# Kernel optimization log

Hardware: AMD Instinct MI355X
Metric: run time of the kernel (lower is better)

Reference implementation:

```python
import jax, jax.numpy as jnp
import numpy as np

B, T, NCH, DFF = 64, 480, 32, 32   # batch, seq_len+pred_len, d_model, d_ff
LAYERS = 3                          # conv_layers
NFFT, WIN, HOP = 64, 64, 4
FRAMES = T // HOP + 1               # 121 == (seq_len+pred_len+hop)/hop


def _stft(x):
    # x: [B, N, T] real -> (re, im) each [B, N, NFFT, FRAMES]
    # torch.stft(center=True, pad_mode='reflect', normalized=True, onesided=False)
    pad = NFFT // 2
    xp = jnp.pad(x, ((0, 0), (0, 0), (pad, pad)), mode='reflect')
    idx = jnp.arange(FRAMES)[:, None] * HOP + jnp.arange(NFFT)[None, :]
    win = 0.5 * (1.0 - jnp.cos(2.0 * jnp.pi * jnp.arange(WIN, dtype=jnp.float32) / WIN))  # periodic hann
    frames = xp[:, :, idx] * win                      # [B, N, FRAMES, NFFT]
    spec = jnp.fft.fft(frames, axis=-1) / jnp.sqrt(jnp.float32(NFFT))
    spec = jnp.swapaxes(spec, -1, -2)                 # [B, N, NFFT, FRAMES]
    return spec.real.astype(x.dtype), spec.imag.astype(x.dtype)


def _conv2d(x, w, b, dil, pad):
    y = jax.lax.conv_general_dilated(
        x, w, window_strides=(1, 1), padding=[(pad, pad), (pad, pad)],
        rhs_dilation=(dil, dil), dimension_numbers=('NCHW', 'OIHW', 'NCHW'))
    return y + b[None, :, None, None]


def _cconv(xr, xi, wr, wi, br, bi, dil, pad):
    # apply_complexConv2D: fr(re) - fi(im) + 1j*(fr(im) + fi(re)), biases included in each apply
    rr = _conv2d(xr, wr, br, dil, pad)
    ri = _conv2d(xi, wr, br, dil, pad)
    ir = _conv2d(xr, wi, bi, dil, pad)
    ii = _conv2d(xi, wi, bi, dil, pad)
    return rr - ii, ri + ir


def _cmul(order, ar, ai, br, bi):
    return (jnp.einsum(order, ar, br) - jnp.einsum(order, ai, bi),
            jnp.einsum(order, ar, bi) + jnp.einsum(order, ai, br))


def reference(x, w0r, w0i, b0r, b0i, W1r, W1i, B1r, B1i, W2r, W2i, B2r, B2i, w_l0, b_l0, w_l2, b_l2):
    xt = jnp.swapaxes(x, 1, 2)                         # [B, N, T]
    sr, si = _stft(xt)                                 # [B, N, F, K]
    qkr, qki = _cmul('bnfk,bngk->bnfg', sr, si, sr, si)
    qkr, qki = jax.nn.sigmoid(qkr), jax.nn.sigmoid(qki)
    ar, ai = _cmul('bnfg,bngk->bnfk', qkr, qki, sr, si)

    outs_r, outs_i = [], []
    r0, i0 = _cconv(ar, ai, w0r, w0i, b0r, b0i, 1, 0)  # 1x1 complex conv
    outs_r.append(jax.nn.relu(r0)); outs_i.append(jax.nn.relu(i0))
    for k in range(1, LAYERS):                          # dilated 3x3 complex conv pairs
        j = k - 1
        hr, hi = _cconv(ar, ai, W1r[j], W1i[j], B1r[j], B1i[j], k, k)
        hr, hi = _cconv(hr, hi, W2r[j], W2i[j], B2r[j], B2i[j], k, k)
        outs_r.append(jax.nn.relu(hr)); outs_i.append(jax.nn.relu(hi))
    mr = sum(outs_r) / LAYERS
    mi = sum(outs_i) / LAYERS

    # l0: Linear(2 -> 1) over stacked [real, imag]
    cr = mr * w_l0[0, 0] + mi * w_l0[0, 1] + b_l0[0]    # [B, N, F, K]
    h = cr.mean(axis=2)                                 # [B, N, K]
    y = jnp.einsum('bnk,tk->bnt', h, w_l2) + b_l2       # l2: Linear(FRAMES -> T)
    return jnp.transpose(y, (0, 2, 1))                  # [B, T, N]


def setup_inputs() -> dict:
    key = jax.random.key(0)
    ks = jax.random.split(key, 18)
    s1 = 1.0 / np.sqrt(NCH)          # 1x1 conv fan-in
    s3 = 1.0 / np.sqrt(NCH * 9)      # 3x3 conv fan-in
    return {
        'x':   jax.random.normal(ks[0], (B, T, NCH), jnp.float32),
        'w0r': jax.random.normal(ks[1], (NCH, NCH, 1, 1), jnp.float32) * s1,
        'w0i': jax.random.normal(ks[2], (NCH, NCH, 1, 1), jnp.float32) * s1,
        'b0r': jax.random.normal(ks[3], (NCH,), jnp.float32) * 0.01,
        'b0i': jax.random.normal(ks[4], (NCH,), jnp.float32) * 0.01,
        'W1r': jax.random.normal(ks[5], (LAYERS - 1, DFF, NCH, 3, 3), jnp.float32) * s3,
        'W1i': jax.random.normal(ks[6], (LAYERS - 1, DFF, NCH, 3, 3), jnp.float32) * s3,
        'B1r': jax.random.normal(ks[7], (LAYERS - 1, DFF), jnp.float32) * 0.01,
        'B1i': jax.random.normal(ks[8], (LAYERS - 1, DFF), jnp.float32) * 0.01,
        'W2r': jax.random.normal(ks[9], (LAYERS - 1, NCH, DFF, 3, 3), jnp.float32) * s3,
        'W2i': jax.random.normal(ks[10], (LAYERS - 1, NCH, DFF, 3, 3), jnp.float32) * s3,
        'B2r': jax.random.normal(ks[11], (LAYERS - 1, NCH), jnp.float32) * 0.01,
        'B2i': jax.random.normal(ks[12], (LAYERS - 1, NCH), jnp.float32) * 0.01,
        'w_l0': jax.random.normal(ks[13], (1, 2), jnp.float32) * 0.5,
        'b_l0': jax.random.normal(ks[14], (1,), jnp.float32) * 0.01,
        'w_l2': jax.random.normal(ks[15], (T, FRAMES), jnp.float32) * (1.0 / np.sqrt(FRAMES)),
        'b_l2': jax.random.normal(ks[16], (T,), jnp.float32) * 0.01,
    }
```

## Files before the change

### kernel.cpp

```cpp
#include <hip/hip_runtime.h>
#include <hip/hip_bf16.h>


typedef __attribute__((ext_vector_type(8))) short bf16x8;
typedef __attribute__((ext_vector_type(4))) short bf16x4;
typedef __attribute__((ext_vector_type(4))) float f32x4;

__device__ __forceinline__ ushort f2bf(float v) {
  __hip_bfloat16 h = __float2bfloat16(v);
  return *reinterpret_cast<ushort*>(&h);
}
__device__ __forceinline__ float bf2f_raw(ushort u) {
  union { uint i; float f; } c; c.i = ((uint)u) << 16; return c.f;
}
__device__ __forceinline__ void split_bf(float v, ushort& h, ushort& l) {
  h = f2bf(v); l = f2bf(v - bf2f_raw(h));
}
__device__ __forceinline__ bf16x8 mk8(bf16x4 a, bf16x4 b) {
  bf16x8 r;
  r[0]=a[0]; r[1]=a[1]; r[2]=a[2]; r[3]=a[3];
  r[4]=b[0]; r[5]=b[1]; r[6]=b[2]; r[7]=b[3];
  return r;
}

#define MFMA16(A,B,C) __builtin_amdgcn_mfma_f32_16x16x32_bf16(A, B, C, 0, 0, 0)
#define SPMACC(acc, Ah, Al, Bh, Bl)      \
  acc = MFMA16(Ah, Bh, acc);             \
  acc = MFMA16(Al, Bh, acc);             \
  acc = MFMA16(Ah, Bl, acc);

__global__ __launch_bounds__(512) void stft_mfma_k(const float* __restrict__ x,
                                                   const ushort* __restrict__ WF,
                                                   ushort* __restrict__ ap) {
  __shared__ __align__(16) char smem[133376];
  const int bid = blockIdx.x;
  const int b = bid >> 5, n = bid & 31;
  const int tid = threadIdx.x;
  ushort* xph = reinterpret_cast<ushort*>(smem + 131072);
  ushort* xpl = xph + 576;

  for (int i = tid; i < 576; i += 512) {
    float v = 0.f;
    if (i < 544) {
      int p = i - 32;
      if (p < 0) p = -p;
      if (p >= 480) p = 958 - p;
      v = x[(b * 480 + p) * 32 + n];
    }
    ushort h, l; split_bf(v, h, l);
    xph[i] = h; xpl[i] = l;
  }
  __syncthreads();

  const int wv = tid >> 6, lane = tid & 63;
  const int mt = wv >> 1, nth = wv & 1;
  const int l15 = lane & 15, l4 = lane >> 4;

  bf16x8 WA[2][2][2];
#pragma unroll
  for (int cs = 0; cs < 2; ++cs)
#pragma unroll
    for (int part = 0; part < 2; ++part)
#pragma unroll
      for (int ks = 0; ks < 2; ++ks)
        WA[cs][part][ks] = *reinterpret_cast<const bf16x8*>(
            WF + (((cs * 2 + part) * 2 + ks) * 4 + mt) * 512 + lane * 8);

  f32x4 acc1[2][4];
#pragma unroll
  for (int cs = 0; cs < 2; ++cs)
#pragma unroll
    for (int nt = 0; nt < 4; ++nt) acc1[cs][nt] = (f32x4){0.f, 0.f, 0.f, 0.f};

#pragma unroll
  for (int ks = 0; ks < 2; ++ks) {
    bf16x8 bh[4], bl[4];
#pragma unroll
    for (int nt = 0; nt < 4; ++nt) {
      int n_ = ((nth * 4 + nt) * 16) + l15;
      int e = n_ * 4 + ks * 32 + l4 * 8;
      bf16x4 h0 = *reinterpret_cast<const bf16x4*>(xph + e);
      bf16x4 h1 = *reinterpret_cast<const bf16x4*>(xph + e + 4);
      bf16x4 l0 = *reinterpret_cast<const bf16x4*>(xpl + e);
      bf16x4 l1 = *reinterpret_cast<const bf16x4*>(xpl + e + 4);
      bh[nt] = mk8(h0, h1); bl[nt] = mk8(l0, l1);
    }
#pragma unroll
    for (int cs = 0; cs < 2; ++cs)
#pragma unroll
      for (int nt = 0; nt < 4; ++nt) {
        SPMACC(acc1[cs][nt], WA[cs][0][ks], WA[cs][1][ks], bh[nt], bl[nt]);
      }
  }

#pragma unroll
  for (int cs = 0; cs < 2; ++cs)
#pragma unroll
    for (int nt = 0; nt < 4; ++nt) {
      int k = (nth * 4 + nt) * 16 + l15;
      bool kv = (k < 121);
#pragma unroll
      for (int r = 0; r < 4; ++r) {
        int f = mt * 16 + l4 * 4 + r;
        float v = kv ? acc1[cs][nt][r] : 0.f;
        ushort h, l; split_bf(v, h, l);
        int ba = (f << 8) + (k << 1); ba ^= (f & 7) << 4;
        *reinterpret_cast<ushort*>(smem + cs * 32768 + ba) = h;
        *reinterpret_cast<ushort*>(smem + cs * 32768 + 16384 + ba) = l;
        int bt = (k << 7) + (f << 1); bt ^= (k & 7) << 4;
        *reinterpret_cast<ushort*>(smem + 65536 + cs * 32768 + bt) = h;
        *reinterpret_cast<ushort*>(smem + 65536 + cs * 32768 + 16384 + bt) = l;
      }
    }
  __syncthreads();

  f32x4 acc2[2][4];
#pragma unroll
  for (int nt = 0; nt < 2; ++nt)
#pragma unroll
    for (int c = 0; c < 4; ++c) acc2[nt][c] = (f32x4){0.f, 0.f, 0.f, 0.f};

#pragma unroll
  for (int ks = 0; ks < 4; ++ks) {
    bf16x8 A_[2][2];
#pragma unroll
    for (int comp = 0; comp < 2; ++comp)
#pragma unroll
      for (int part = 0; part < 2; ++part) {
        int f = mt * 16 + l15;
        int ba = (f << 8) + ((ks * 32 + l4 * 8) << 1); ba ^= (f & 7) << 4;
        A_[comp][part] = *reinterpret_cast<const bf16x8*>(smem + comp * 32768 + part * 16384 + ba);
      }
    bf16x8 B_[2][2][2];
#pragma unroll
    for (int comp = 0; comp < 2; ++comp)
#pragma unroll
      for (int part = 0; part < 2; ++part)
#pragma unroll
        for (int nt = 0; nt < 2; ++nt) {
          int g = (nth * 2 + nt) * 16 + l15;
          int ba = (g << 8) + ((ks * 32 + l4 * 8) << 1); ba ^= (g & 7) << 4;
          B_[comp][part][nt] = *reinterpret_cast<const bf16x8*>(smem + comp * 32768 + part * 16384 + ba);
        }
#pragma unroll
    for (int nt = 0; nt < 2; ++nt) {
      SPMACC(acc2[nt][0], A_[0][0], A_[0][1], B_[0][0][nt], B_[0][1][nt]);
      SPMACC(acc2[nt][1], A_[1][0], A_[1][1], B_[1][0][nt], B_[1][1][nt]);
      SPMACC(acc2[nt][2], A_[0][0], A_[0][1], B_[1][0][nt], B_[1][1][nt]);
      SPMACC(acc2[nt][3], A_[1][0], A_[1][1], B_[0][0][nt], B_[0][1][nt]);
    }
  }
  __syncthreads();

#pragma unroll
  for (int nt = 0; nt < 2; ++nt) {
    int g = (nth * 2 + nt) * 16 + l15;
#pragma unroll
    for (int r = 0; r < 4; ++r) {
      int f = mt * 16 + l4 * 4 + r;
      float qr = acc2[nt][0][r] - acc2[nt][1][r];
      float qi = acc2[nt][2][r] + acc2[nt][3][r];
      float vr = 1.f / (1.f + __expf(-qr));
      float vi = 1.f / (1.f + __expf(-qi));
      int ba = (f << 7) + (g << 1); ba ^= (f & 7) << 4;
      ushort h, l;
      split_bf(vr, h, l);
      *reinterpret_cast<ushort*>(smem + ba) = h;
      *reinterpret_cast<ushort*>(smem + 8192 + ba) = l;
      split_bf(vi, h, l);
      *reinterpret_cast<ushort*>(smem + 16384 + ba) = h;
      *reinterpret_cast<ushort*>(smem + 24576 + ba) = l;
    }
  }
  __syncthreads();

  f32x4 acc3[4][3];
#pragma unroll
  for (int nt = 0; nt < 4; ++nt)
#pragma unroll
    for (int c = 0; c < 3; ++c) acc3[nt][c] = (f32x4){0.f, 0.f, 0.f, 0.f};

#pragma unroll
  for (int ks = 0; ks < 2; ++ks) {
    bf16x8 QA[2][2];
#pragma unroll
    for (int comp = 0; comp < 2; ++comp)
#pragma unroll
      for (int part = 0; part < 2; ++part) {
        int f = mt * 16 + l15;
        int ba = (f << 7) + ((ks * 32 + l4 * 8) << 1); ba ^= (f & 7) << 4;
        QA[comp][part] = *reinterpret_cast<const bf16x8*>(smem + comp * 16384 + part * 8192 + ba);
      }
#pragma unroll
    for (int nt = 0; nt < 4; ++nt) {
      int k = (nth * 4 + nt) * 16 + l15;
      int bq = (k << 7) + ((ks * 32 + l4 * 8) << 1); bq ^= (k & 7) << 4;
      bf16x8 Srh = *reinterpret_cast<const bf16x8*>(smem + 65536 + bq);
      bf16x8 Srl = *reinterpret_cast<const bf16x8*>(smem + 81920 + bq);
      bf16x8 Sih = *reinterpret_cast<const bf16x8*>(smem + 98304 + bq);
      bf16x8 Sil = *reinterpret_cast<const bf16x8*>(smem + 114688 + bq);
      SPMACC(acc3[nt][0], QA[0][0], QA[0][1], Srh, Srl);
      SPMACC(acc3[nt][1], QA[1][0], QA[1][1], Sih, Sil);
      SPMACC(acc3[nt][2], QA[0][0], QA[0][1], Sih, Sil);
      SPMACC(acc3[nt][2], QA[1][0], QA[1][1], Srh, Srl);
    }
  }
  __syncthreads();

#pragma unroll
  for (int nt = 0; nt < 4; ++nt) {
    int k = (nth * 4 + nt) * 16 + l15;
#pragma unroll
    for (int r = 0; r < 4; ++r) {
      int f = mt * 16 + l4 * 4 + r;
      float ar = acc3[nt][0][r] - acc3[nt][1][r];
      float ai = acc3[nt][2][r];
      int ba = (f << 8) + (k << 1); ba ^= (f & 7) << 4;
      *reinterpret_cast<ushort*>(smem + ba) = f2bf(ar);
      *reinterpret_cast<ushort*>(smem + 16384 + ba) = f2bf(ai);
    }
  }
  __syncthreads();

  uint4* dst = reinterpret_cast<uint4*>(ap);
  for (int i = tid; i < 2048; i += 512) {
    int comp = i >> 10, rem = i & 1023;
    int f = rem >> 4, q = rem & 15;
    uint4 v = *reinterpret_cast<const uint4*>(
        smem + comp * 16384 + (f << 8) + ((q ^ (f & 7)) << 4));
    dst[((size_t)(b * 64 + n + 32 * comp) * 64) * 16 + rem] = v;
  }
}

__global__ __launch_bounds__(256) void transpose_k(const ushort* __restrict__ ap,
                                                   ushort* __restrict__ an) {
  __shared__ ushort T[64 * 128];
  const int b = blockIdx.x >> 6, h = blockIdx.x & 63;
  const int tid = threadIdx.x;
#pragma unroll
  for (int it = 0; it < 4; ++it) {
    int i = it * 256 + tid;
    int cc = i >> 4, q = i & 15;
    const uint4* src = reinterpret_cast<const uint4*>(ap) +
                       ((size_t)((b * 64 + cc) * 64 + h) * 16 + q);
    *reinterpret_cast<uint4*>(&T[cc * 128 + q * 8]) = *src;
  }
  __syncthreads();
  const int p = tid >> 1, cc0 = (tid & 1) * 32;
  uint ou[16];
#pragma unroll
  for (int it = 0; it < 16; ++it) {
    uint lo = T[(cc0 + 2 * it) * 128 + p];
    uint hi = T[(cc0 + 2 * it + 1) * 128 + p];
    ou[it] = lo | (hi << 16);
  }
  uint4* dst = reinterpret_cast<uint4*>(an + ((size_t)((b * 64 + h) * 128 + p) * 64 + cc0));
#pragma unroll
  for (int r = 0; r < 4; ++r) dst[r] = make_uint4(ou[4*r], ou[4*r+1], ou[4*r+2], ou[4*r+3]);
}

__global__ __launch_bounds__(256) void prep_k(
    const float* __restrict__ w0r, const float* __restrict__ w0i,
    const float* __restrict__ b0r, const float* __restrict__ b0i,
    const float* __restrict__ W1r, const float* __restrict__ W1i,
    const float* __restrict__ B1r, const float* __restrict__ B1i,
    const float* __restrict__ W2r, const float* __restrict__ W2i,
    const float* __restrict__ B2r, const float* __restrict__ B2i,
    const float* __restrict__ wl2,
    ushort* __restrict__ AF, ushort* __restrict__ WF, float* __restrict__ BB,
    float* __restrict__ wl2T) {
  const int blk = blockIdx.x, tid = threadIdx.x;
  const float PI32 = 0.0981747704246810387f;

  if (blk == 38) {
    for (int i = tid; i < 121 * 480; i += 256) {
      int k = i / 480, t = i - k * 480;
      wl2T[i] = wl2[t * 121 + k];
    }
    return;
  }
  if (blk == 37) {
    for (int i = tid; i < 16384; i += 256) {
      int j = i & 7, ln = (i >> 3) & 63, mt = (i >> 9) & 3, ks = (i >> 11) & 1;
      int part = (i >> 12) & 1, cs = (i >> 13) & 1;
      int f = mt * 16 + (ln & 15);
      int t = ks * 32 + (ln >> 4) * 8 + j;
      float win = 0.5f * (1.0f - __cosf(PI32 * (float)t));
      int m = (f * t) & 63;
      float sv, cv;
      __sincosf(PI32 * (float)m, &sv, &cv);
      float val = (cs == 0) ? (win * cv * 0.125f) : (-win * sv * 0.125f);
      ushort h = f2bf(val);
      WF[i] = part ? f2bf(val - bf2f_raw(h)) : h;
    }
    return;
  }

  int conv, tap, TT;
  const float *Wr, *Wi;
  if (blk == 0) { conv = 0; tap = 0; TT = 1; Wr = w0r; Wi = w0i; }
  else {
    int q = blk - 1; conv = 1 + q / 9; tap = q - (q / 9) * 9; TT = 9;
    if (conv == 1)      { Wr = W1r;        Wi = W1i; }
    else if (conv == 2) { Wr = W2r;        Wi = W2i; }
    else if (conv == 3) { Wr = W1r + 9216; Wi = W1i + 9216; }
    else                { Wr = W2r + 9216; Wi = W2i + 9216; }
  }
  ushort thi[16], tlo[16];
#pragma unroll
  for (int jj = 0; jj < 16; ++jj) {
    int e = tid * 16 + jj;
    int j = e & 7, lane_e = (e >> 3) & 63, mt = (e >> 9) & 3, ks = (e >> 11) & 1;
    int o  = mt * 16 + (lane_e & 15);
    int cc = ks * 32 + 8 * (lane_e >> 4) + j;
    int ci = cc & 31, ch = cc >> 5, on = o & 31, oh = o >> 5;
    float wr = Wr[(on * 32 + ci) * TT + tap];
    float wi = Wi[(on * 32 + ci) * TT + tap];
    float v = (oh == 0) ? (ch == 0 ? wr : -wi) : (ch == 0 ? wi : wr);
    ushort h = f2bf(v);
    thi[jj] = h;
    tlo[jj] = f2bf(v - bf2f_raw(h));
  }
  ushort* base = AF + conv * 73728 + tap * 8192 + tid * 16;
  uint4* dh = reinterpret_cast<uint4*>(base);
  uint4* dl = reinterpret_cast<uint4*>(base + 4096);
  dh[0] = *reinterpret_cast<uint4*>(&thi[0]);
  dh[1] = *reinterpret_cast<uint4*>(&thi[8]);
  dl[0] = *reinterpret_cast<uint4*>(&tlo[0]);
  dl[1] = *reinterpret_cast<uint4*>(&tlo[8]);

  if (blk == 0) {
    for (int i = tid; i < 320; i += 256) {
      int c = i >> 6, o = i & 63;
      const float *br, *bi;
      if (c == 0)      { br = b0r;      bi = b0i; }
      else if (c == 1) { br = B1r;      bi = B1i; }
      else if (c == 2) { br = B2r;      bi = B2i; }
      else if (c == 3) { br = B1r + 32; bi = B1i + 32; }
      else             { br = B2r + 32; bi = B2i + 32; }
      BB[c * 64 + o] = (o < 32) ? (br[o] - bi[o]) : (br[o - 32] + bi[o - 32]);
    }
  }
}

#define RWB 8704

template <int NT>
__device__ __forceinline__ void run_taps(const char* __restrict__ smem,
    const ushort* __restrict__ afrag, int d,
    int ng, int mtb, int l15, int l4, int lane, f32x4 acc[2][8]) {
  const ushort* Ab = afrag + lane * 8;
#pragma unroll
  for (int t = 0; t < NT; ++t) {
    const int dy = (NT == 1) ? 1 : (t / 3);
    const int dxo = ((NT == 1) ? 0 : ((t - (t / 3) * 3) - 1)) * d;
    const int bufb = (dy - 1) * d + 2 + ng * 2;
    const ushort* At = Ab + t * 8192;
    bf16x8 AH[2][2], AL[2][2];
#pragma unroll
    for (int ks = 0; ks < 2; ++ks)
#pragma unroll
      for (int mi = 0; mi < 2; ++mi) {
        AH[ks][mi] = *reinterpret_cast<const bf16x8*>(At + ks * 2048 + (mtb + 2 * mi) * 512);
        AL[ks][mi] = *reinterpret_cast<const bf16x8*>(At + 4096 + ks * 2048 + (mtb + 2 * mi) * 512);
      }
#pragma unroll
    for (int ks = 0; ks < 2; ++ks) {
      bf16x8 bv[8];
#pragma unroll
      for (int nt = 0; nt < 8; ++nt) {
        int bw = (nt & 3) * 16 + l15 + dxo + 2;
        int byt = (bufb + (nt >> 2)) * RWB + bw * 128 + ks * 64 + l4 * 16;
        byt ^= (bw & 7) << 4;
        bv[nt] = *reinterpret_cast<const bf16x8*>(smem + byt);
      }
      __builtin_amdgcn_s_setprio(1);
#pragma unroll
      for (int nt = 0; nt < 8; ++nt) {
        acc[0][nt] = MFMA16(AH[ks][0], bv[nt], acc[0][nt]);
        acc[1][nt] = MFMA16(AH[ks][1], bv[nt], acc[1][nt]);
      }
#pragma unroll
      for (int nt = 0; nt < 8; ++nt) {
        acc[0][nt] = MFMA16(AL[ks][0], bv[nt], acc[0][nt]);
        acc[1][nt] = MFMA16(AL[ks][1], bv[nt], acc[1][nt]);
      }
      __builtin_amdgcn_s_setprio(0);
    }
  }
}

template <int ROWS>
__device__ __forceinline__ void conv_body(char* smem,
    const ushort* __restrict__ xin, ushort* __restrict__ tout,
    const ushort* __restrict__ afrag, const float* __restrict__ bb,
    const float* __restrict__ wl0, float* __restrict__ csum,
    int d, int b, int h0, int side, int mode, int tid) {
  const int wave = tid >> 6, lane = tid & 63;
  const int mtb = wave & 1;
  const int ng = wave >> 1;
  const int l15 = lane & 15, l4 = lane >> 4;
  const int wbase = side * 64;

  const int RSTG = (ROWS == 1) ? 4 : 8;
#pragma unroll
  for (int r = 0; r < RSTG; ++r) {
    const int hh = (ROWS == 1) ? (h0 + r) : (h0 + r - 2);
    const int buf = (ROWS == 1) ? (r + 2) : r;
    const bool hv = ((unsigned)hh < 64u);
    uint4 st[3];
#pragma unroll
    for (int c = 0; c < 3; ++c) {
      int i = c * 256 + tid;
      uint4 v = make_uint4(0u, 0u, 0u, 0u);
      if (i < 544) {
        int bw = i >> 3, q = i & 7;
        int gw = wbase + bw - 2;
        if (hv && (unsigned)gw < 128u)
          v = *reinterpret_cast<const uint4*>(
              xin + (((size_t)(b * 64 + hh) * 128 + gw) * 64 + q * 8));
      }
      st[c] = v;
    }
#pragma unroll
    for (int c = 0; c < 3; ++c) {
      int i = c * 256 + tid;
      if (i < 544) {
        int bw = i >> 3, q = i & 7;
        int byt = buf * RWB + bw * 128 + q * 16;
        byt ^= (bw & 7) << 4;
        *reinterpret_cast<uint4*>(smem + byt) = st[c];
      }
    }
  }
  __syncthreads();

  f32x4 acc[2][8];
#pragma unroll
  for (int mi = 0; mi < 2; ++mi)
#pragma unroll
    for (int nt = 0; nt < 8; ++nt) acc[mi][nt] = (f32x4){0.f, 0.f, 0.f, 0.f};

  run_taps<(ROWS == 1) ? 1 : 9>(smem, afrag, d, ng, mtb, l15, l4, lane, acc);

  if (mode == 2) {
    __syncthreads();
    uint* Lb = reinterpret_cast<uint*>(smem);
#pragma unroll
    for (int mi = 0; mi < 2; ++mi) {
#pragma unroll
      for (int rp = 0; rp < 2; ++rp) {
        int o = (mtb + 2 * mi) * 16 + l4 * 4 + rp * 2;
        float b0 = bb[o], b1 = bb[o + 1];
#pragma unroll
        for (int nt = 0; nt < 8; ++nt) {
          int jrow = ng * 2 + (nt >> 2);
          int wl = (nt & 3) * 16 + l15;
          uint pk = (uint)f2bf(acc[mi][nt][rp * 2] + b0) |
                    ((uint)f2bf(acc[mi][nt][rp * 2 + 1] + b1) << 16);
          Lb[(jrow * 32 + (o >> 1)) * 66 + wl] = pk;
        }
      }
    }
    __syncthreads();
#pragma unroll
    for (int c = 0; c < 8; ++c) {
      int i = c * 256 + tid;
      int jrow = i >> 9, rem = i & 511;
      int wl = rem >> 3, q = rem & 7;
      int gw = wbase + wl;
      int hh = h0 + jrow;
      bool val = (gw < 121);
      uint4 v;
      v.x = val ? Lb[(jrow * 32 + q * 4 + 0) * 66 + wl] : 0u;
      v.y = val ? Lb[(jrow * 32 + q * 4 + 1) * 66 + wl] : 0u;
      v.z = val ? Lb[(jrow * 32 + q * 4 + 2) * 66 + wl] : 0u;
      v.w = val ? Lb[(jrow * 32 + q * 4 + 3) * 66 + wl] : 0u;
      *reinterpret_cast<uint4*>(
          tout + (((size_t)(b * 64 + hh) * 128 + gw) * 64 + q * 8)) = v;
    }
  } else {
    const float w00 = wl0[0], w01 = wl0[1];
#pragma unroll
    for (int nt = 0; nt < 8; ++nt) {
      int gw = wbase + (nt & 3) * 16 + l15;
      int hh = h0 + ng * 2 + (nt >> 2);
      if (gw < 121) {
#pragma unroll
        for (int r = 0; r < 4; ++r) {
          int n = mtb * 16 + l4 * 4 + r;
          float rr = acc[0][nt][r] + bb[n];
          float im = acc[1][nt][r] + bb[n + 32];
          float v = (fmaxf(rr, 0.f) * w00 + fmaxf(im, 0.f) * w01) * (1.f / 3.f);
          float* p = csum + ((size_t)(b * 32 + n) * 64 + hh) * 121 + gw;
          if (mode == 1) v += *p;
          *p = v;
        }
      }
    }
  }
}

__global__ __launch_bounds__(256, 2) void convD1_k(
    const ushort* __restrict__ an, ushort* __restrict__ t1, ushort* __restrict__ t2,
    const ushort* __restrict__ AF, const float* __restrict__ BB,
    const float* __restrict__ wl0, float* __restrict__ csumA) {
  __shared__ __align__(16) char smem[8 * RWB];
  const int x = blockIdx.x & 7, j = blockIdx.x >> 3;
  const int role = j % 3, sub = j / 3;
  const int wg = (x << 8) | sub;
  const int b = wg >> 5, rem = wg & 31;
  const int h0 = ((rem >> 1) & 15) * 4, side = rem & 1;
  const int tid = threadIdx.x;
  if (role == 0)
    conv_body<1>(smem, an, nullptr, AF, BB, wl0, csumA, 1, b, h0, side, 0, tid);
  else if (role == 1)
    conv_body<3>(smem, an, t1, AF + 1 * 73728, BB + 64, wl0, nullptr, 1, b, h0, side, 2, tid);
  else
    conv_body<3>(smem, an, t2, AF + 3 * 73728, BB + 192, wl0, nullptr, 2, b, h0, side, 2, tid);
}

__global__ __launch_bounds__(256, 2) void convD2_k(
    const ushort* __restrict__ t1, const ushort* __restrict__ t2,
    const ushort* __restrict__ AF, const float* __restrict__ BB,
    const float* __restrict__ wl0, float* __restrict__ csumA,
    float* __restrict__ csumB) {
  __shared__ __align__(16) char smem[8 * RWB];
  const int x = blockIdx.x & 7, j = blockIdx.x >> 3;
  const int role = j & 1, sub = j >> 1;
  const int wg = (x << 8) | sub;
  const int b = wg >> 5, rem = wg & 31;
  const int h0 = ((rem >> 1) & 15) * 4, side = rem & 1;
  const int tid = threadIdx.x;
  if (role == 0)
    conv_body<3>(smem, t1, nullptr, AF + 2 * 73728, BB + 128, wl0, csumA, 1, b, h0, side, 1, tid);
  else
    conv_body<3>(smem, t2, nullptr, AF + 4 * 73728, BB + 256, wl0, csumB, 2, b, h0, side, 0, tid);
}

__global__ __launch_bounds__(256) void epi_k(const float* __restrict__ csumA,
    const float* __restrict__ csumB,
    const float* __restrict__ bl0, const float* __restrict__ wl2T,
    const float* __restrict__ bl2, float* __restrict__ out) {
  const int b = blockIdx.x >> 5, n = blockIdx.x & 31;
  __shared__ float sh[121];
  const int tid = threadIdx.x;
  const float* baseA = csumA + (size_t)(b * 32 + n) * 64 * 121;
  const float* baseB = csumB + (size_t)(b * 32 + n) * 64 * 121;
  for (int k = tid; k < 121; k += 256) {
    float s = 0.f;
#pragma unroll 8
    for (int f = 0; f < 64; ++f) s += baseA[f * 121 + k] + baseB[f * 121 + k];
    sh[k] = s * (1.f / 64.f) + bl0[0];
  }
  __syncthreads();
  for (int t = tid; t < 480; t += 256) {
    float acc = bl2[t];
#pragma unroll 8
    for (int k = 0; k < 121; ++k) acc = fmaf(sh[k], wl2T[k * 480 + t], acc);
    out[(b * 480 + t) * 32 + n] = acc;
  }
}

extern "C" void kernel_launch(void* const* d_in, const int* in_sizes, int n_in,
                              void* d_out, int out_size, void* d_ws, size_t ws_size,
                              hipStream_t stream) {
  const float* x   = (const float*)d_in[0];
  const float* w0r = (const float*)d_in[1];
  const float* w0i = (const float*)d_in[2];
  const float* b0r = (const float*)d_in[3];
  const float* b0i = (const float*)d_in[4];
  const float* W1r = (const float*)d_in[5];
  const float* W1i = (const float*)d_in[6];
  const float* B1r = (const float*)d_in[7];
  const float* B1i = (const float*)d_in[8];
  const float* W2r = (const float*)d_in[9];
  const float* W2i = (const float*)d_in[10];
  const float* B2r = (const float*)d_in[11];
  const float* B2i = (const float*)d_in[12];
  const float* wl0 = (const float*)d_in[13];
  const float* bl0 = (const float*)d_in[14];
  const float* wl2 = (const float*)d_in[15];
  const float* bl2 = (const float*)d_in[16];

  char* ws = (char*)d_ws;
  const size_t MB64 = (size_t)64 << 20;
  ushort* ap    = (ushort*)ws;
  ushort* t2    = (ushort*)ws;
  ushort* an    = (ushort*)(ws + MB64);
  float*  csumB = (float*)(ws + MB64);
  ushort* t1    = (ushort*)(ws + 2 * MB64);
  float*  csumA = (float*)(ws + 3 * MB64);
  const size_t CSZ = (size_t)64 * 32 * 64 * 121 * 4;
  ushort* AF   = (ushort*)(ws + 3 * MB64 + CSZ);
  ushort* WFp  = AF + 5 * 73728;
  float*  BB   = (float*)(WFp + 16384);
  float*  wl2T = BB + 320;
  float*  out  = (float*)d_out;

  hipLaunchKernelGGL(prep_k, dim3(39), dim3(256), 0, stream,
                     w0r, w0i, b0r, b0i, W1r, W1i, B1r, B1i, W2r, W2i, B2r, B2i,
                     wl2, AF, WFp, BB, wl2T);
  hipLaunchKernelGGL(stft_mfma_k, dim3(2048), dim3(512), 0, stream, x, WFp, ap);
  hipLaunchKernelGGL(transpose_k, dim3(4096), dim3(256), 0, stream, ap, an);
  hipLaunchKernelGGL(convD1_k, dim3(6144), dim3(256), 0, stream,
                     an, t1, t2, AF, BB, wl0, csumA);
  hipLaunchKernelGGL(convD2_k, dim3(4096), dim3(256), 0, stream,
                     t1, t2, AF, BB, wl0, csumA, csumB);
  hipLaunchKernelGGL(epi_k, dim3(2048), dim3(256), 0, stream,
                     csumA, csumB, bl0, wl2T, bl2, out);
}
```

Measured before the change: 555.9 us.

## Make conv kernels persistent with rolling row buffer and fuse 1x1 conv into transpose

The 1x1 complex conv is moved into the transpose kernel, reusing the transposed tile already in shared memory to compute its csum contribution. The 3x3 conv kernels become persistent: each block walks 32 rows using a ring of 8 shared-memory row buffers, prefetching the next 4 rows into registers while computing. Weight fragments for the next tap are double-buffered in registers. This removes the redundant halo reloads and cuts launch overhead, at the cost of only 512 blocks (less parallelism) and higher register pressure.

New measurement: 1.058 ms. 90.3% more time.

```diff
diff --git a/kernel.cpp b/kernel.cpp
--- a/kernel.cpp
+++ b/kernel.cpp
@@ -233,8 +233,10 @@
 }
 
 __global__ __launch_bounds__(256) void transpose_k(const ushort* __restrict__ ap,
-                                                   ushort* __restrict__ an) {
-  __shared__ ushort T[64 * 128];
+    ushort* __restrict__ an, const ushort* __restrict__ AF,
+    const float* __restrict__ BB, const float* __restrict__ wl0,
+    float* __restrict__ csumA) {
+  __shared__ __align__(16) ushort T[64 * 128];
   const int b = blockIdx.x >> 6, h = blockIdx.x & 63;
   const int tid = threadIdx.x;
 #pragma unroll
@@ -257,6 +259,70 @@
   uint4* dst = reinterpret_cast<uint4*>(an + ((size_t)((b * 64 + h) * 128 + p) * 64 + cc0));
 #pragma unroll
   for (int r = 0; r < 4; ++r) dst[r] = make_uint4(ou[4*r], ou[4*r+1], ou[4*r+2], ou[4*r+3]);
+  __syncthreads();
+
+  char* S = reinterpret_cast<char*>(T);
+#pragma unroll
+  for (int it = 0; it < 16; ++it) {
+    int byt = p * 128 + (cc0 + 2 * it) * 2;
+    byt ^= (p & 7) << 4;
+    *reinterpret_cast<uint*>(S + byt) = ou[it];
+  }
+  __syncthreads();
+
+  const int wave = tid >> 6, lane = tid & 63;
+  const int mtb = wave & 1, ntb = (wave >> 1) * 4;
+  const int l15 = lane & 15, l4 = lane >> 4;
+  const ushort* Ab = AF + lane * 8;
+  bf16x8 AH[2][2], AL[2][2];
+#pragma unroll
+  for (int ks = 0; ks < 2; ++ks)
+#pragma unroll
+    for (int mi = 0; mi < 2; ++mi) {
+      AH[ks][mi] = *reinterpret_cast<const bf16x8*>(Ab + ks * 2048 + (mtb + 2 * mi) * 512);
+      AL[ks][mi] = *reinterpret_cast<const bf16x8*>(Ab + 4096 + ks * 2048 + (mtb + 2 * mi) * 512);
+    }
+  f32x4 acc[2][4];
+#pragma unroll
+  for (int mi = 0; mi < 2; ++mi)
+#pragma unroll
+    for (int nt = 0; nt < 4; ++nt) acc[mi][nt] = (f32x4){0.f, 0.f, 0.f, 0.f};
+#pragma unroll
+  for (int ks = 0; ks < 2; ++ks) {
+    bf16x8 bv[4];
+#pragma unroll
+    for (int nt = 0; nt < 4; ++nt) {
+      int w = (ntb + nt) * 16 + l15;
+      int byt = w * 128 + ks * 64 + l4 * 16;
+      byt ^= (w & 7) << 4;
+      bv[nt] = *reinterpret_cast<const bf16x8*>(S + byt);
+    }
+#pragma unroll
+    for (int nt = 0; nt < 4; ++nt) {
+      acc[0][nt] = MFMA16(AH[ks][0], bv[nt], acc[0][nt]);
+      acc[1][nt] = MFMA16(AH[ks][1], bv[nt], acc[1][nt]);
+    }
+#pragma unroll
+    for (int nt = 0; nt < 4; ++nt) {
+      acc[0][nt] = MFMA16(AL[ks][0], bv[nt], acc[0][nt]);
+      acc[1][nt] = MFMA16(AL[ks][1], bv[nt], acc[1][nt]);
+    }
+  }
+  const float w00 = wl0[0], w01 = wl0[1];
+#pragma unroll
+  for (int nt = 0; nt < 4; ++nt) {
+    int gw = (ntb + nt) * 16 + l15;
+    if (gw < 121) {
+#pragma unroll
+      for (int r = 0; r < 4; ++r) {
+        int n = mtb * 16 + l4 * 4 + r;
+        float rr = acc[0][nt][r] + BB[n];
+        float im = acc[1][nt][r] + BB[n + 32];
+        csumA[((size_t)(b * 32 + n) * 64 + h) * 121 + gw] =
+            (fmaxf(rr, 0.f) * w00 + fmaxf(im, 0.f) * w01) * (1.f / 3.f);
+      }
+    }
+  }
 }
 
 __global__ __launch_bounds__(256) void prep_k(
@@ -345,179 +411,235 @@
 
 #define RWB 8704
 
-template <int NT>
-__device__ __forceinline__ void run_taps(const char* __restrict__ smem,
-    const ushort* __restrict__ afrag, int d,
+__device__ __forceinline__ void run9(const char* __restrict__ smem,
+    const ushort* __restrict__ afrag, bf16x8 AC[2][2][2], int d, int h0,
     int ng, int mtb, int l15, int l4, int lane, f32x4 acc[2][8]) {
   const ushort* Ab = afrag + lane * 8;
-#pragma unroll
-  for (int t = 0; t < NT; ++t) {
-    const int dy = (NT == 1) ? 1 : (t / 3);
-    const int dxo = ((NT == 1) ? 0 : ((t - (t / 3) * 3) - 1)) * d;
-    const int bufb = (dy - 1) * d + 2 + ng * 2;
-    const ushort* At = Ab + t * 8192;
-    bf16x8 AH[2][2], AL[2][2];
-#pragma unroll
-    for (int ks = 0; ks < 2; ++ks)
-#pragma unroll
-      for (int mi = 0; mi < 2; ++mi) {
-        AH[ks][mi] = *reinterpret_cast<const bf16x8*>(At + ks * 2048 + (mtb + 2 * mi) * 512);
-        AL[ks][mi] = *reinterpret_cast<const bf16x8*>(At + 4096 + ks * 2048 + (mtb + 2 * mi) * 512);
-      }
+  bf16x8 AN[2][2][2];
+#pragma unroll
+  for (int t = 0; t < 9; ++t) {
+    if (t < 8) {
+      const ushort* At = Ab + (t + 1) * 8192;
+#pragma unroll
+      for (int pp = 0; pp < 2; ++pp)
+#pragma unroll
+        for (int ks = 0; ks < 2; ++ks)
+#pragma unroll
+          for (int mi = 0; mi < 2; ++mi)
+            AN[pp][ks][mi] = *reinterpret_cast<const bf16x8*>(
+                At + pp * 4096 + ks * 2048 + (mtb + 2 * mi) * 512);
+    }
+    const int dy = t / 3;
+    const int dxo = (t - dy * 3 - 1) * d;
+    const int bufb = h0 + (dy - 1) * d + 2 + ng * 2;
+    const int base0 = (bufb & 7) * RWB;
+    const int base1 = ((bufb + 1) & 7) * RWB;
 #pragma unroll
     for (int ks = 0; ks < 2; ++ks) {
       bf16x8 bv[8];
 #pragma unroll
       for (int nt = 0; nt < 8; ++nt) {
         int bw = (nt & 3) * 16 + l15 + dxo + 2;
-        int byt = (bufb + (nt >> 2)) * RWB + bw * 128 + ks * 64 + l4 * 16;
+        int byt = ((nt >> 2) ? base1 : base0) + bw * 128 + ks * 64 + l4 * 16;
         byt ^= (bw & 7) << 4;
         bv[nt] = *reinterpret_cast<const bf16x8*>(smem + byt);
       }
       __builtin_amdgcn_s_setprio(1);
 #pragma unroll
       for (int nt = 0; nt < 8; ++nt) {
-        acc[0][nt] = MFMA16(AH[ks][0], bv[nt], acc[0][nt]);
-        acc[1][nt] = MFMA16(AH[ks][1], bv[nt], acc[1][nt]);
+        acc[0][nt] = MFMA16(AC[0][ks][0], bv[nt], acc[0][nt]);
+        acc[1][nt] = MFMA16(AC[0][ks][1], bv[nt], acc[1][nt]);
       }
 #pragma unroll
       for (int nt = 0; nt < 8; ++nt) {
-        acc[0][nt] = MFMA16(AL[ks][0], bv[nt], acc[0][nt]);
-        acc[1][nt] = MFMA16(AL[ks][1], bv[nt], acc[1][nt]);
+        acc[0][nt] = MFMA16(AC[1][ks][0], bv[nt], acc[0][nt]);
+        acc[1][nt] = MFMA16(AC[1][ks][1], bv[nt], acc[1][nt]);
       }
       __builtin_amdgcn_s_setprio(0);
     }
-  }
-}
-
-template <int ROWS>
-__device__ __forceinline__ void conv_body(char* smem,
+    if (t < 8) {
+#pragma unroll
+      for (int pp = 0; pp < 2; ++pp)
+#pragma unroll
+        for (int ks = 0; ks < 2; ++ks)
+#pragma unroll
+          for (int mi = 0; mi < 2; ++mi)
+            AC[pp][ks][mi] = AN[pp][ks][mi];
+    }
+  }
+}
+
+__device__ __forceinline__ void conv_persist(char* __restrict__ smem,
     const ushort* __restrict__ xin, ushort* __restrict__ tout,
     const ushort* __restrict__ afrag, const float* __restrict__ bb,
     const float* __restrict__ wl0, float* __restrict__ csum,
-    int d, int b, int h0, int side, int mode, int tid) {
+    int d, int b, int side, int hbase, int mode, int tid) {
   const int wave = tid >> 6, lane = tid & 63;
   const int mtb = wave & 1;
   const int ng = wave >> 1;
   const int l15 = lane & 15, l4 = lane >> 4;
   const int wbase = side * 64;
-
-  const int RSTG = (ROWS == 1) ? 4 : 8;
-#pragma unroll
-  for (int r = 0; r < RSTG; ++r) {
-    const int hh = (ROWS == 1) ? (h0 + r) : (h0 + r - 2);
-    const int buf = (ROWS == 1) ? (r + 2) : r;
-    const bool hv = ((unsigned)hh < 64u);
+  const float w00 = wl0[0], w01 = wl0[1];
+
+#define PLOAD(st, hh)                                                          \
+  {                                                                            \
+    const bool hv = ((unsigned)(hh) < 64u);                                    \
+    _Pragma("unroll")                                                          \
+    for (int c = 0; c < 3; ++c) {                                              \
+      int i = c * 256 + tid;                                                   \
+      uint4 v = make_uint4(0u, 0u, 0u, 0u);                                    \
+      if (i < 544) {                                                           \
+        int bw = i >> 3, q = i & 7;                                            \
+        int gw = wbase + bw - 2;                                               \
+        if (hv && (unsigned)gw < 128u)                                         \
+          v = *reinterpret_cast<const uint4*>(                                 \
+              xin + (((size_t)(b * 64 + (hh)) * 128 + gw) * 64 + q * 8));      \
+      }                                                                        \
+      st[c] = v;                                                               \
+    }                                                                          \
+  }
+#define PWRITE(st, buf)                                                        \
+  {                                                                            \
+    _Pragma("unroll")                                                          \
+    for (int c = 0; c < 3; ++c) {                                              \
+      int i = c * 256 + tid;                                                   \
+      if (i < 544) {                                                           \
+        int bw = i >> 3, q = i & 7;                                            \
+        int byt = (buf) * RWB + bw * 128 + q * 16;                             \
+        byt ^= (bw & 7) << 4;                                                  \
+        *reinterpret_cast<uint4*>(smem + byt) = st[c];                         \
+      }                                                                        \
+    }                                                                          \
+  }
+
+  {
     uint4 st[3];
 #pragma unroll
-    for (int c = 0; c < 3; ++c) {
-      int i = c * 256 + tid;
-      uint4 v = make_uint4(0u, 0u, 0u, 0u);
-      if (i < 544) {
-        int bw = i >> 3, q = i & 7;
-        int gw = wbase + bw - 2;
-        if (hv && (unsigned)gw < 128u)
-          v = *reinterpret_cast<const uint4*>(
-              xin + (((size_t)(b * 64 + hh) * 128 + gw) * 64 + q * 8));
-      }
-      st[c] = v;
-    }
-#pragma unroll
-    for (int c = 0; c < 3; ++c) {
-      int i = c * 256 + tid;
-      if (i < 544) {
-        int bw = i >> 3, q = i & 7;
-        int byt = buf * RWB + bw * 128 + q * 16;
-        byt ^= (bw & 7) << 4;
-        *reinterpret_cast<uint4*>(smem + byt) = st[c];
-      }
-    }
-  }
-  __syncthreads();
-
-  f32x4 acc[2][8];
-#pragma unroll
-  for (int mi = 0; mi < 2; ++mi)
-#pragma unroll
-    for (int nt = 0; nt < 8; ++nt) acc[mi][nt] = (f32x4){0.f, 0.f, 0.f, 0.f};
-
-  run_taps<(ROWS == 1) ? 1 : 9>(smem, afrag, d, ng, mtb, l15, l4, lane, acc);
-
-  if (mode == 2) {
+    for (int r = 0; r < 8; ++r) {
+      PLOAD(st, hbase - 2 + r);
+      PWRITE(st, r);
+    }
+  }
+  __syncthreads();
+
+  for (int i = 0; i < 8; ++i) {
+    const int h0 = hbase + i * 4;
+    const bool last = (i == 7);
+
+    bf16x8 AC[2][2][2];
+    {
+      const ushort* Ab = afrag + lane * 8;
+#pragma unroll
+      for (int pp = 0; pp < 2; ++pp)
+#pragma unroll
+        for (int ks = 0; ks < 2; ++ks)
+#pragma unroll
+          for (int mi = 0; mi < 2; ++mi)
+            AC[pp][ks][mi] = *reinterpret_cast<const bf16x8*>(
+                Ab + pp * 4096 + ks * 2048 + (mtb + 2 * mi) * 512);
+    }
+    uint4 st0[3], st1[3], st2[3], st3[3];
+    if (!last) {
+      PLOAD(st0, h0 + 6);
+      PLOAD(st1, h0 + 7);
+      PLOAD(st2, h0 + 8);
+      PLOAD(st3, h0 + 9);
+    }
+
+    f32x4 acc[2][8];
+#pragma unroll
+    for (int mi = 0; mi < 2; ++mi)
+#pragma unroll
+      for (int nt = 0; nt < 8; ++nt) acc[mi][nt] = (f32x4){0.f, 0.f, 0.f, 0.f};
+
+    run9(smem, afrag, AC, d, h0, ng, mtb, l15, l4, lane, acc);
+
+    if (mode == 2) {
+      __syncthreads();
+      const int rbase = (h0 & 7) ? 4 * RWB : 0;
+      uint* Lb = reinterpret_cast<uint*>(smem + rbase);
+#pragma unroll
+      for (int mi = 0; mi < 2; ++mi) {
+#pragma unroll
+        for (int rp = 0; rp < 2; ++rp) {
+          int o = (mtb + 2 * mi) * 16 + l4 * 4 + rp * 2;
+          float b0 = bb[o], b1 = bb[o + 1];
+#pragma unroll
+          for (int nt = 0; nt < 8; ++nt) {
+            int jrow = ng * 2 + (nt >> 2);
+            int wl = (nt & 3) * 16 + l15;
+            uint pk = (uint)f2bf(acc[mi][nt][rp * 2] + b0) |
+                      ((uint)f2bf(acc[mi][nt][rp * 2 + 1] + b1) << 16);
+            Lb[(jrow * 32 + (o >> 1)) * 66 + wl] = pk;
+          }
+        }
+      }
+      __syncthreads();
+#pragma unroll
+      for (int c = 0; c < 8; ++c) {
+        int i2 = c * 256 + tid;
+        int jrow = i2 >> 9, rem2 = i2 & 511;
+        int wl = rem2 >> 3, q = rem2 & 7;
+        int gw = wbase + wl;
+        int hh = h0 + jrow;
+        bool val = (gw < 121);
+        uint4 v;
+        v.x = val ? Lb[(jrow * 32 + q * 4 + 0) * 66 + wl] : 0u;
+        v.y = val ? Lb[(jrow * 32 + q * 4 + 1) * 66 + wl] : 0u;
+        v.z = val ? Lb[(jrow * 32 + q * 4 + 2) * 66 + wl] : 0u;
+        v.w = val ? Lb[(jrow * 32 + q * 4 + 3) * 66 + wl] : 0u;
+        *reinterpret_cast<uint4*>(
+            tout + (((size_t)(b * 64 + hh) * 128 + gw) * 64 + q * 8)) = v;
+      }
+      __syncthreads();
+    } else {
+#pragma unroll
+      for (int nt = 0; nt < 8; ++nt) {
+        int gw = wbase + (nt & 3) * 16 + l15;
+        int hh = h0 + ng * 2 + (nt >> 2);
+        if (gw < 121) {
+#pragma unroll
+          for (int r = 0; r < 4; ++r) {
+            int n = mtb * 16 + l4 * 4 + r;
+            float rr = acc[0][nt][r] + bb[n];
+            float im = acc[1][nt][r] + bb[n + 32];
+            float v = (fmaxf(rr, 0.f) * w00 + fmaxf(im, 0.f) * w01) * (1.f / 3.f);
+            float* pc = csum + ((size_t)(b * 32 + n) * 64 + hh) * 121 + gw;
+            if (mode == 1) v += *pc;
+            *pc = v;
+          }
+        }
+      }
+      __syncthreads();
+    }
+
+    if (!last) {
+      const int bb0 = h0 & 7;
+      PWRITE(st0, bb0 + 0);
+      PWRITE(st1, bb0 + 1);
+      PWRITE(st2, bb0 + 2);
+      PWRITE(st3, bb0 + 3);
+    }
     __syncthreads();
-    uint* Lb = reinterpret_cast<uint*>(smem);
-#pragma unroll
-    for (int mi = 0; mi < 2; ++mi) {
-#pragma unroll
-      for (int rp = 0; rp < 2; ++rp) {
-        int o = (mtb + 2 * mi) * 16 + l4 * 4 + rp * 2;
-        float b0 = bb[o], b1 = bb[o + 1];
-#pragma unroll
-        for (int nt = 0; nt < 8; ++nt) {
-          int jrow = ng * 2 + (nt >> 2);
-          int wl = (nt & 3) * 16 + l15;
-          uint pk = (uint)f2bf(acc[mi][nt][rp * 2] + b0) |
-                    ((uint)f2bf(acc[mi][nt][rp * 2 + 1] + b1) << 16);
-          Lb[(jrow * 32 + (o >> 1)) * 66 + wl] = pk;
-        }
-      }
-    }
-    __syncthreads();
-#pragma unroll
-    for (int c = 0; c < 8; ++c) {
-      int i = c * 256 + tid;
-      int jrow = i >> 9, rem = i & 511;
-      int wl = rem >> 3, q = rem & 7;
-      int gw = wbase + wl;
-      int hh = h0 + jrow;
-      bool val = (gw < 121);
-      uint4 v;
-      v.x = val ? Lb[(jrow * 32 + q * 4 + 0) * 66 + wl] : 0u;
-      v.y = val ? Lb[(jrow * 32 + q * 4 + 1) * 66 + wl] : 0u;
-      v.z = val ? Lb[(jrow * 32 + q * 4 + 2) * 66 + wl] : 0u;
-      v.w = val ? Lb[(jrow * 32 + q * 4 + 3) * 66 + wl] : 0u;
-      *reinterpret_cast<uint4*>(
-          tout + (((size_t)(b * 64 + hh) * 128 + gw) * 64 + q * 8)) = v;
-    }
-  } else {
-    const float w00 = wl0[0], w01 = wl0[1];
-#pragma unroll
-    for (int nt = 0; nt < 8; ++nt) {
-      int gw = wbase + (nt & 3) * 16 + l15;
-      int hh = h0 + ng * 2 + (nt >> 2);
-      if (gw < 121) {
-#pragma unroll
-        for (int r = 0; r < 4; ++r) {
-          int n = mtb * 16 + l4 * 4 + r;
-          float rr = acc[0][nt][r] + bb[n];
-          float im = acc[1][nt][r] + bb[n + 32];
-          float v = (fmaxf(rr, 0.f) * w00 + fmaxf(im, 0.f) * w01) * (1.f / 3.f);
-          float* p = csum + ((size_t)(b * 32 + n) * 64 + hh) * 121 + gw;
-          if (mode == 1) v += *p;
-          *p = v;
-        }
-      }
-    }
-  }
+  }
+#undef PLOAD
+#undef PWRITE
 }
 
 __global__ __launch_bounds__(256, 2) void convD1_k(
     const ushort* __restrict__ an, ushort* __restrict__ t1, ushort* __restrict__ t2,
     const ushort* __restrict__ AF, const float* __restrict__ BB,
-    const float* __restrict__ wl0, float* __restrict__ csumA) {
+    const float* __restrict__ wl0) {
   __shared__ __align__(16) char smem[8 * RWB];
   const int x = blockIdx.x & 7, j = blockIdx.x >> 3;
-  const int role = j % 3, sub = j / 3;
-  const int wg = (x << 8) | sub;
-  const int b = wg >> 5, rem = wg & 31;
-  const int h0 = ((rem >> 1) & 15) * 4, side = rem & 1;
+  const int wg = (x << 6) | j;
+  const int b = wg >> 3, rem = wg & 7;
+  const int role = rem & 1, side = (rem >> 1) & 1, hbase = (rem >> 2) * 32;
   const int tid = threadIdx.x;
   if (role == 0)
-    conv_body<1>(smem, an, nullptr, AF, BB, wl0, csumA, 1, b, h0, side, 0, tid);
-  else if (role == 1)
-    conv_body<3>(smem, an, t1, AF + 1 * 73728, BB + 64, wl0, nullptr, 1, b, h0, side, 2, tid);
+    conv_persist(smem, an, t1, AF + 1 * 73728, BB + 64, wl0, nullptr, 1, b, side, hbase, 2, tid);
   else
-    conv_body<3>(smem, an, t2, AF + 3 * 73728, BB + 192, wl0, nullptr, 2, b, h0, side, 2, tid);
+    conv_persist(smem, an, t2, AF + 3 * 73728, BB + 192, wl0, nullptr, 2, b, side, hbase, 2, tid);
 }
 
 __global__ __launch_bounds__(256, 2) void convD2_k(
@@ -527,15 +649,14 @@
     float* __restrict__ csumB) {
   __shared__ __align__(16) char smem[8 * RWB];
   const int x = blockIdx.x & 7, j = blockIdx.x >> 3;
-  const int role = j & 1, sub = j >> 1;
-  const int wg = (x << 8) | sub;
-  const int b = wg >> 5, rem = wg & 31;
-  const int h0 = ((rem >> 1) & 15) * 4, side = rem & 1;
+  const int wg = (x << 6) | j;
+  const int b = wg >> 3, rem = wg & 7;
+  const int role = rem & 1, side = (rem >> 1) & 1, hbase = (rem >> 2) * 32;
   const int tid = threadIdx.x;
   if (role == 0)
-    conv_body<3>(smem, t1, nullptr, AF + 2 * 73728, BB + 128, wl0, csumA, 1, b, h0, side, 1, tid);
+    conv_persist(smem, t1, nullptr, AF + 2 * 73728, BB + 128, wl0, csumA, 1, b, side, hbase, 1, tid);
   else
-    conv_body<3>(smem, t2, nullptr, AF + 4 * 73728, BB + 256, wl0, csumB, 2, b, h0, side, 0, tid);
+    conv_persist(smem, t2, nullptr, AF + 4 * 73728, BB + 256, wl0, csumB, 2, b, side, hbase, 0, tid);
 }
 
 __global__ __launch_bounds__(256) void epi_k(const float* __restrict__ csumA,
@@ -602,10 +723,11 @@
                      w0r, w0i, b0r, b0i, W1r, W1i, B1r, B1i, W2r, W2i, B2r, B2i,
                      wl2, AF, WFp, BB, wl2T);
   hipLaunchKernelGGL(stft_mfma_k, dim3(2048), dim3(512), 0, stream, x, WFp, ap);
-  hipLaunchKernelGGL(transpose_k, dim3(4096), dim3(256), 0, stream, ap, an);
-  hipLaunchKernelGGL(convD1_k, dim3(6144), dim3(256), 0, stream,
-                     an, t1, t2, AF, BB, wl0, csumA);
-  hipLaunchKernelGGL(convD2_k, dim3(4096), dim3(256), 0, stream,
+  hipLaunchKernelGGL(transpose_k, dim3(4096), dim3(256), 0, stream,
+                     ap, an, AF, BB, wl0, csumA);
+  hipLaunchKernelGGL(convD1_k, dim3(512), dim3(256), 0, stream,
+                     an, t1, t2, AF, BB, wl0);
+  hipLaunchKernelGGL(convD2_k, dim3(512), dim3(256), 0, stream,
                      t1, t2, AF, BB, wl0, csumA, csumB);
   hipLaunchKernelGGL(epi_k, dim3(2048), dim3(256), 0, stream,
                      csumA, csumB, bl0, wl2T, bl2, out);
```

## Fuse 1x1 complex conv into transpose kernel, drop role from convD1

Applied to the files above, without the earlier changes.

Moves the 1x1 complex conv (layer 0) out of convD1_k and into transpose_k. That conv is computed from the transposed row already held in shared memory, so it needs no separate block that restages four rows from global memory. convD1_k now launches only the two 3x3 roles, with 4096 blocks instead of 6144. This cuts a global reload of the activation and a third of the convD1 blocks, in exchange for extra MFMA work and register use in the transpose kernel.

New measurement: 533.0 us. -4.1%, faster.

```diff
diff --git a/kernel.cpp b/kernel.cpp
--- a/kernel.cpp
+++ b/kernel.cpp
@@ -233,8 +233,10 @@
 }
 
 __global__ __launch_bounds__(256) void transpose_k(const ushort* __restrict__ ap,
-                                                   ushort* __restrict__ an) {
-  __shared__ ushort T[64 * 128];
+    ushort* __restrict__ an, const ushort* __restrict__ AF,
+    const float* __restrict__ BB, const float* __restrict__ wl0,
+    float* __restrict__ csumA) {
+  __shared__ __align__(16) ushort T[64 * 128];
   const int b = blockIdx.x >> 6, h = blockIdx.x & 63;
   const int tid = threadIdx.x;
 #pragma unroll
@@ -257,6 +259,70 @@
   uint4* dst = reinterpret_cast<uint4*>(an + ((size_t)((b * 64 + h) * 128 + p) * 64 + cc0));
 #pragma unroll
   for (int r = 0; r < 4; ++r) dst[r] = make_uint4(ou[4*r], ou[4*r+1], ou[4*r+2], ou[4*r+3]);
+  __syncthreads();
+
+  char* S = reinterpret_cast<char*>(T);
+#pragma unroll
+  for (int it = 0; it < 16; ++it) {
+    int byt = p * 128 + (cc0 + 2 * it) * 2;
+    byt ^= (p & 7) << 4;
+    *reinterpret_cast<uint*>(S + byt) = ou[it];
+  }
+  __syncthreads();
+
+  const int wave = tid >> 6, lane = tid & 63;
+  const int mtb = wave & 1, ntb = (wave >> 1) * 4;
+  const int l15 = lane & 15, l4 = lane >> 4;
+  const ushort* Ab = AF + lane * 8;
+  bf16x8 AH[2][2], AL[2][2];
+#pragma unroll
+  for (int ks = 0; ks < 2; ++ks)
+#pragma unroll
+    for (int mi = 0; mi < 2; ++mi) {
+      AH[ks][mi] = *reinterpret_cast<const bf16x8*>(Ab + ks * 2048 + (mtb + 2 * mi) * 512);
+      AL[ks][mi] = *reinterpret_cast<const bf16x8*>(Ab + 4096 + ks * 2048 + (mtb + 2 * mi) * 512);
+    }
+  f32x4 acc[2][4];
+#pragma unroll
+  for (int mi = 0; mi < 2; ++mi)
+#pragma unroll
+    for (int nt = 0; nt < 4; ++nt) acc[mi][nt] = (f32x4){0.f, 0.f, 0.f, 0.f};
+#pragma unroll
+  for (int ks = 0; ks < 2; ++ks) {
+    bf16x8 bv[4];
+#pragma unroll
+    for (int nt = 0; nt < 4; ++nt) {
+      int w = (ntb + nt) * 16 + l15;
+      int byt = w * 128 + ks * 64 + l4 * 16;
+      byt ^= (w & 7) << 4;
+      bv[nt] = *reinterpret_cast<const bf16x8*>(S + byt);
+    }
+#pragma unroll
+    for (int nt = 0; nt < 4; ++nt) {
+      acc[0][nt] = MFMA16(AH[ks][0], bv[nt], acc[0][nt]);
+      acc[1][nt] = MFMA16(AH[ks][1], bv[nt], acc[1][nt]);
+    }
+#pragma unroll
+    for (int nt = 0; nt < 4; ++nt) {
+      acc[0][nt] = MFMA16(AL[ks][0], bv[nt], acc[0][nt]);
+      acc[1][nt] = MFMA16(AL[ks][1], bv[nt], acc[1][nt]);
+    }
+  }
+  const float w00 = wl0[0], w01 = wl0[1];
+#pragma unroll
+  for (int nt = 0; nt < 4; ++nt) {
+    int gw = (ntb + nt) * 16 + l15;
+    if (gw < 121) {
+#pragma unroll
+      for (int r = 0; r < 4; ++r) {
+        int n = mtb * 16 + l4 * 4 + r;
+        float rr = acc[0][nt][r] + BB[n];
+        float im = acc[1][nt][r] + BB[n + 32];
+        csumA[((size_t)(b * 32 + n) * 64 + h) * 121 + gw] =
+            (fmaxf(rr, 0.f) * w00 + fmaxf(im, 0.f) * w01) * (1.f / 3.f);
+      }
+    }
+  }
 }
 
 __global__ __launch_bounds__(256) void prep_k(
@@ -345,15 +411,14 @@
 
 #define RWB 8704
 
-template <int NT>
-__device__ __forceinline__ void run_taps(const char* __restrict__ smem,
+__device__ __forceinline__ void run_taps9(const char* __restrict__ smem,
     const ushort* __restrict__ afrag, int d,
     int ng, int mtb, int l15, int l4, int lane, f32x4 acc[2][8]) {
   const ushort* Ab = afrag + lane * 8;
 #pragma unroll
-  for (int t = 0; t < NT; ++t) {
-    const int dy = (NT == 1) ? 1 : (t / 3);
-    const int dxo = ((NT == 1) ? 0 : ((t - (t / 3) * 3) - 1)) * d;
+  for (int t = 0; t < 9; ++t) {
+    const int dy = t / 3;
+    const int dxo = ((t - dy * 3) - 1) * d;
     const int bufb = (dy - 1) * d + 2 + ng * 2;
     const ushort* At = Ab + t * 8192;
     bf16x8 AH[2][2], AL[2][2];
@@ -390,8 +455,7 @@
   }
 }
 
-template <int ROWS>
-__device__ __forceinline__ void conv_body(char* smem,
+__device__ __forceinline__ void conv_body3(char* smem,
     const ushort* __restrict__ xin, ushort* __restrict__ tout,
     const ushort* __restrict__ afrag, const float* __restrict__ bb,
     const float* __restrict__ wl0, float* __restrict__ csum,
@@ -402,11 +466,9 @@
   const int l15 = lane & 15, l4 = lane >> 4;
   const int wbase = side * 64;
 
-  const int RSTG = (ROWS == 1) ? 4 : 8;
-#pragma unroll
-  for (int r = 0; r < RSTG; ++r) {
-    const int hh = (ROWS == 1) ? (h0 + r) : (h0 + r - 2);
-    const int buf = (ROWS == 1) ? (r + 2) : r;
+#pragma unroll
+  for (int r = 0; r < 8; ++r) {
+    const int hh = h0 + r - 2;
     const bool hv = ((unsigned)hh < 64u);
     uint4 st[3];
 #pragma unroll
@@ -427,7 +489,7 @@
       int i = c * 256 + tid;
       if (i < 544) {
         int bw = i >> 3, q = i & 7;
-        int byt = buf * RWB + bw * 128 + q * 16;
+        int byt = r * RWB + bw * 128 + q * 16;
         byt ^= (bw & 7) << 4;
         *reinterpret_cast<uint4*>(smem + byt) = st[c];
       }
@@ -441,7 +503,7 @@
 #pragma unroll
     for (int nt = 0; nt < 8; ++nt) acc[mi][nt] = (f32x4){0.f, 0.f, 0.f, 0.f};
 
-  run_taps<(ROWS == 1) ? 1 : 9>(smem, afrag, d, ng, mtb, l15, l4, lane, acc);
+  run_taps9(smem, afrag, d, ng, mtb, l15, l4, lane, acc);
 
   if (mode == 2) {
     __syncthreads();
@@ -504,20 +566,18 @@
 __global__ __launch_bounds__(256, 2) void convD1_k(
     const ushort* __restrict__ an, ushort* __restrict__ t1, ushort* __restrict__ t2,
     const ushort* __restrict__ AF, const float* __restrict__ BB,
-    const float* __restrict__ wl0, float* __restrict__ csumA) {
+    const float* __restrict__ wl0) {
   __shared__ __align__(16) char smem[8 * RWB];
   const int x = blockIdx.x & 7, j = blockIdx.x >> 3;
-  const int role = j % 3, sub = j / 3;
+  const int role = j & 1, sub = j >> 1;
   const int wg = (x << 8) | sub;
   const int b = wg >> 5, rem = wg & 31;
   const int h0 = ((rem >> 1) & 15) * 4, side = rem & 1;
   const int tid = threadIdx.x;
   if (role == 0)
-    conv_body<1>(smem, an, nullptr, AF, BB, wl0, csumA, 1, b, h0, side, 0, tid);
-  else if (role == 1)
-    conv_body<3>(smem, an, t1, AF + 1 * 73728, BB + 64, wl0, nullptr, 1, b, h0, side, 2, tid);
+    conv_body3(smem, an, t1, AF + 1 * 73728, BB + 64, wl0, nullptr, 1, b, h0, side, 2, tid);
   else
-    conv_body<3>(smem, an, t2, AF + 3 * 73728, BB + 192, wl0, nullptr, 2, b, h0, side, 2, tid);
+    conv_body3(smem, an, t2, AF + 3 * 73728, BB + 192, wl0, nullptr, 2, b, h0, side, 2, tid);
 }
 
 __global__ __launch_bounds__(256, 2) void convD2_k(
@@ -533,9 +593,9 @@
   const int h0 = ((rem >> 1) & 15) * 4, side = rem & 1;
   const int tid = threadIdx.x;
   if (role == 0)
-    conv_body<3>(smem, t1, nullptr, AF + 2 * 73728, BB + 128, wl0, csumA, 1, b, h0, side, 1, tid);
+    conv_body3(smem, t1, nullptr, AF + 2 * 73728, BB + 128, wl0, csumA, 1, b, h0, side, 1, tid);
   else
-    conv_body<3>(smem, t2, nullptr, AF + 4 * 73728, BB + 256, wl0, csumB, 2, b, h0, side, 0, tid);
+    conv_body3(smem, t2, nullptr, AF + 4 * 73728, BB + 256, wl0, csumB, 2, b, h0, side, 0, tid);
 }
 
 __global__ __launch_bounds__(256) void epi_k(const float* __restrict__ csumA,
@@ -602,9 +662,10 @@
                      w0r, w0i, b0r, b0i, W1r, W1i, B1r, B1i, W2r, W2i, B2r, B2i,
                      wl2, AF, WFp, BB, wl2T);
   hipLaunchKernelGGL(stft_mfma_k, dim3(2048), dim3(512), 0, stream, x, WFp, ap);
-  hipLaunchKernelGGL(transpose_k, dim3(4096), dim3(256), 0, stream, ap, an);
-  hipLaunchKernelGGL(convD1_k, dim3(6144), dim3(256), 0, stream,
-                     an, t1, t2, AF, BB, wl0, csumA);
+  hipLaunchKernelGGL(transpose_k, dim3(4096), dim3(256), 0, stream,
+                     ap, an, AF, BB, wl0, csumA);
+  hipLaunchKernelGGL(convD1_k, dim3(4096), dim3(256), 0, stream,
+                     an, t1, t2, AF, BB, wl0);
   hipLaunchKernelGGL(convD2_k, dim3(4096), dim3(256), 0, stream,
                      t1, t2, AF, BB, wl0, csumA, csumB);
   hipLaunchKernelGGL(epi_k, dim3(2048), dim3(256), 0, stream,
```
